# Kernel tuning notes

Measured on AMD Instinct MI355X. Metric: run time of the kernel, lower is better.

Reference implementation:

```python
import jax, jax.numpy as jnp
import numpy as np

EMBED = 768
HIDDEN = 768
HEADS = 12
HEAD_DIM = HIDDEN // HEADS
B, S = 4, 2048


def setup_inputs() -> dict:
    key = jax.random.key(0)
    ks = jax.random.split(key, 12)
    sd = 1.0 / np.sqrt(EMBED)
    return {
        "vector1": jax.random.normal(ks[0], (B, S, EMBED), jnp.float32),
        "vector2": jax.random.normal(ks[1], (B, S, EMBED), jnp.float32),
        "Wq": jax.random.normal(ks[2], (HIDDEN, EMBED), jnp.float32) * sd,
        "bq": jnp.zeros((HIDDEN,), jnp.float32),
        "Wk": jax.random.normal(ks[3], (HIDDEN, EMBED), jnp.float32) * sd,
        "bk": jnp.zeros((HIDDEN,), jnp.float32),
        "Wv": jax.random.normal(ks[4], (HIDDEN, EMBED), jnp.float32) * sd,
        "bv": jnp.zeros((HIDDEN,), jnp.float32),
        "Wo": jax.random.normal(ks[5], (EMBED, HIDDEN), jnp.float32) * sd,
        "bo": jnp.zeros((EMBED,), jnp.float32),
        "alpha": jnp.float32(0.5),
        "beta": jnp.float32(0.5),
    }


def reference(vector1, vector2, Wq, bq, Wk, bk, Wv, bv, Wo, bo, alpha, beta):
    b, s, _ = vector1.shape
    # Linear projections (torch Linear: x @ W.T + b)
    Q = (vector1 @ Wq.T + bq).reshape(b, s, HEADS, HEAD_DIM)  # [B,S,H,D]
    K = (vector2 @ Wk.T + bk).reshape(b, s, HEADS, HEAD_DIM)
    V = (vector2 @ Wv.T + bv).reshape(b, s, HEADS, HEAD_DIM)
    # NOTE: module scales by sqrt(hidden_dim), NOT sqrt(head_dim)
    scale = jnp.float32(np.sqrt(HIDDEN))
    scores = jnp.einsum("bqhd,bkhd->bhqk", Q / scale, K)  # [B,H,S,S]
    # max-subtract + softmax == numerically stable softmax
    attn = jax.nn.softmax(scores, axis=-1)
    out = jnp.einsum("bhqk,bkhd->bqhd", attn, V).reshape(b, s, HIDDEN)
    adjusted = vector1 @ Wo.T + bo
    return alpha * out + beta * adjusted
```

## Files before the change

### kernel.cpp

```cpp
#include <hip/hip_runtime.h>
#include <hip/hip_bf16.h>

#define LOG2E 1.4426950408889634f

typedef __attribute__((ext_vector_type(4)))  float f32x4;
typedef __attribute__((ext_vector_type(16))) float f32x16;
typedef __attribute__((ext_vector_type(8)))  short s16x8;
typedef __attribute__((ext_vector_type(8)))  unsigned short u16x8_t;
typedef __attribute__((ext_vector_type(4)))  int i32x4;

static __device__ __forceinline__ unsigned short f2b(float f) {
    __hip_bfloat16 h = __float2bfloat16(f);
    return __builtin_bit_cast(unsigned short, h);
}

static __device__ __forceinline__ void gload_lds16(const unsigned short* g, unsigned short* l) {
    __builtin_amdgcn_global_load_lds(
        (const __attribute__((address_space(1))) void*)g,
        (__attribute__((address_space(3))) void*)l, 16, 0, 0);
}

__global__ void cvt_f32_to_bf16(const float* __restrict__ src,
                                unsigned short* __restrict__ dst, int n4) {
    int i = blockIdx.x * blockDim.x + threadIdx.x;
    int stride = gridDim.x * blockDim.x;
    for (; i < n4; i += stride) {
        f32x4 v = reinterpret_cast<const f32x4*>(src)[i];
        ushort4 o;
        o.x = f2b(v.x); o.y = f2b(v.y); o.z = f2b(v.z); o.w = f2b(v.w);
        reinterpret_cast<ushort4*>(dst)[i] = o;
    }
}

__global__ void cvt_weights(const float* __restrict__ wq, const float* __restrict__ wk,
                            const float* __restrict__ wv, const float* __restrict__ wo,
                            unsigned short* __restrict__ dst, int quarter4) {
    int i = blockIdx.x * blockDim.x + threadIdx.x;
    int seg = i / quarter4;
    int j = i - seg * quarter4;
    const float* src = (seg == 0) ? wq : (seg == 1) ? wk : (seg == 2) ? wv : wo;
    f32x4 v = reinterpret_cast<const f32x4*>(src)[j];
    ushort4 o;
    o.x = f2b(v.x); o.y = f2b(v.y); o.z = f2b(v.z); o.w = f2b(v.w);
    reinterpret_cast<ushort4*>(dst)[i] = o;
}

__global__ __launch_bounds__(256) void gemm_qkvo(
    const unsigned short* __restrict__ A1,
    const unsigned short* __restrict__ A2,
    const unsigned short* __restrict__ Wcat,
    const float* __restrict__ bq, const float* __restrict__ bk,
    const float* __restrict__ bv, const float* __restrict__ bo,
    unsigned short* __restrict__ Qb,
    unsigned short* __restrict__ Kb,
    unsigned short* __restrict__ Vtb,
    float* __restrict__ adj,
    float qscale)
{
    __shared__ unsigned short As[128 * 64];
    __shared__ unsigned short Bs[128 * 64];

    const int n0g = blockIdx.x * 128;
    const int seg = blockIdx.x / 6;
    const int n0 = n0g - seg * 768;
    const int m0 = blockIdx.y * 128;
    const unsigned short* A = (seg == 1 || seg == 2) ? A2 : A1;
    const float* bias = (seg == 0) ? bq : (seg == 1) ? bk : (seg == 2) ? bv : bo;

    const int tid = threadIdx.x;
    const int w = tid >> 6, lane = tid & 63;
    const int lg = lane >> 4, lr = lane & 15;
    const int wm = w >> 1, wn = w & 1;
    const int srow = tid >> 3;
    const int scol = (tid & 7) * 8;

    const unsigned short* Ag = A    + (size_t)(m0  + srow) * 768 + scol;
    const unsigned short* Bg = Wcat + (size_t)(n0g + srow) * 768 + scol;
    unsigned short* Al = &As[tid * 8];
    unsigned short* Bl = &Bs[tid * 8];

    f32x4 acc[4][4];
#pragma unroll
    for (int i = 0; i < 4; i++)
#pragma unroll
        for (int j = 0; j < 4; j++) acc[i][j] = f32x4{0.f, 0.f, 0.f, 0.f};

    for (int k0 = 0; k0 < 768; k0 += 64) {
#pragma unroll
        for (int c = 0; c < 4; c++) {
            gload_lds16(Ag + c * 32 * 768 + k0, Al + c * 2048);
            gload_lds16(Bg + c * 32 * 768 + k0, Bl + c * 2048);
        }
        __syncthreads();
#pragma unroll
        for (int kk = 0; kk < 2; ++kk) {
            s16x8 af[4], bf[4];
#pragma unroll
            for (int mi = 0; mi < 4; mi++)
                af[mi] = *reinterpret_cast<const s16x8*>(&As[(wm * 64 + mi * 16 + lr) * 64 + kk * 32 + lg * 8]);
#pragma unroll
            for (int ni = 0; ni < 4; ni++)
                bf[ni] = *reinterpret_cast<const s16x8*>(&Bs[(wn * 64 + ni * 16 + lr) * 64 + kk * 32 + lg * 8]);
#pragma unroll
            for (int mi = 0; mi < 4; mi++)
#pragma unroll
                for (int ni = 0; ni < 4; ni++)
                    acc[mi][ni] = __builtin_amdgcn_mfma_f32_16x16x32_bf16(af[mi], bf[ni], acc[mi][ni], 0, 0, 0);
        }
        __syncthreads();
    }

#pragma unroll
    for (int ni = 0; ni < 4; ni++) {
        int n = n0 + wn * 64 + ni * 16 + lr;
        float bn = bias[n];
#pragma unroll
        for (int mi = 0; mi < 4; mi++) {
#pragma unroll
            for (int i = 0; i < 4; i++) {
                int m = m0 + wm * 64 + mi * 16 + 4 * lg + i;
                float v = acc[mi][ni][i] + bn;
                if (seg == 0) {
                    Qb[(size_t)m * 768 + n] = f2b(v * qscale);
                } else if (seg == 1) {
                    Kb[(size_t)m * 768 + n] = f2b(v);
                } else if (seg == 2) {
                    int bb = m >> 11, ss = m & 2047;
                    Vtb[((size_t)(bb * 768 + n) << 11) + ss] = f2b(v);
                } else {
                    adj[(size_t)m * 768 + n] = v;
                }
            }
        }
    }
}

__global__ __launch_bounds__(256) void attn_fused(
    const unsigned short* __restrict__ Qb,
    const unsigned short* __restrict__ Kb,
    const unsigned short* __restrict__ Vt,
    const float* __restrict__ adj,
    const float* __restrict__ alpha_p,
    const float* __restrict__ beta_p,
    float* __restrict__ out)
{
    __shared__ unsigned short Ksm[128][72];
    __shared__ unsigned short Vsm[64][136];

    const int bh = blockIdx.x;
    const int b = bh / 12, h = bh - 12 * (bh / 12);
    const int tid = threadIdx.x, w = tid >> 6, lane = tid & 63;
    const int ql = lane & 31, hi = lane >> 5;
    const int q0 = blockIdx.y * 128 + w * 32;

    const size_t qbase = ((size_t)(b * 2048 + q0 + ql)) * 768 + h * 64;
    s16x8 qreg[4];
#pragma unroll
    for (int ds = 0; ds < 4; ds++)
        qreg[ds] = *reinterpret_cast<const s16x8*>(Qb + qbase + ds * 16 + hi * 8);

    f32x16 acc[2];
#pragma unroll
    for (int dd = 0; dd < 2; dd++)
#pragma unroll
        for (int r = 0; r < 16; r++) acc[dd][r] = 0.f;
    float l = 0.f;

    const size_t kbase = (size_t)b * 2048 * 768 + (size_t)h * 64;
    const size_t vbase = (size_t)(b * 768 + h * 64) * 2048;

    const int krow = tid >> 3, kc8 = (tid & 7) * 8;
    const int vrow = tid >> 4, vc8 = (tid & 15) * 8;

    u16x8_t kst[4], vst[4];
    auto load_tile = [&](int t0) {
#pragma unroll
        for (int i = 0; i < 4; i++)
            kst[i] = *reinterpret_cast<const u16x8_t*>(Kb + kbase + (size_t)(t0 + i * 32 + krow) * 768 + kc8);
#pragma unroll
        for (int i = 0; i < 4; i++)
            vst[i] = *reinterpret_cast<const u16x8_t*>(Vt + vbase + (size_t)(i * 16 + vrow) * 2048 + t0 + vc8);
    };
    load_tile(0);

#pragma unroll 1
    for (int t0 = 0; t0 < 2048; t0 += 128) {
        __syncthreads();
#pragma unroll
        for (int i = 0; i < 4; i++)
            *reinterpret_cast<u16x8_t*>(&Ksm[i * 32 + krow][kc8]) = kst[i];
#pragma unroll
        for (int i = 0; i < 4; i++)
            *reinterpret_cast<u16x8_t*>(&Vsm[i * 16 + vrow][vc8]) = vst[i];
        __syncthreads();
        if (t0 + 128 < 2048) load_tile(t0 + 128);

#pragma unroll
        for (int kb2 = 0; kb2 < 4; kb2++) {
            f32x16 sc;
#pragma unroll
            for (int r = 0; r < 16; r++) sc[r] = 0.f;
#pragma unroll
            for (int ds = 0; ds < 4; ds++) {
                s16x8 ka = *reinterpret_cast<const s16x8*>(&Ksm[kb2 * 32 + ql][ds * 16 + hi * 8]);
                sc = __builtin_amdgcn_mfma_f32_32x32x16_bf16(ka, qreg[ds], sc, 0, 0, 0);
            }

            float p[16];
#pragma unroll
            for (int r = 0; r < 16; r++) p[r] = __builtin_exp2f(sc[r] * LOG2E);
            {
                float s0 = p[0] + p[1],  s1 = p[2] + p[3],  s2 = p[4] + p[5],  s3 = p[6] + p[7];
                float s4 = p[8] + p[9],  s5 = p[10] + p[11], s6 = p[12] + p[13], s7 = p[14] + p[15];
                float t0a = s0 + s1, t1a = s2 + s3, t2a = s4 + s5, t3a = s6 + s7;
                l += (t0a + t1a) + (t2a + t3a);
            }

            s16x8 pf[2];
            {
                unsigned int a0, b0, a1, b1, a2, b2, a3, b3;
                asm("v_cvt_pk_bf16_f32 %0, %1, %2" : "=v"(a0) : "v"(p[0]),  "v"(p[1]));
                asm("v_cvt_pk_bf16_f32 %0, %1, %2" : "=v"(b0) : "v"(p[4]),  "v"(p[5]));
                asm("v_cvt_pk_bf16_f32 %0, %1, %2" : "=v"(a1) : "v"(p[2]),  "v"(p[3]));
                asm("v_cvt_pk_bf16_f32 %0, %1, %2" : "=v"(b1) : "v"(p[6]),  "v"(p[7]));
                asm("v_cvt_pk_bf16_f32 %0, %1, %2" : "=v"(a2) : "v"(p[8]),  "v"(p[9]));
                asm("v_cvt_pk_bf16_f32 %0, %1, %2" : "=v"(b2) : "v"(p[12]), "v"(p[13]));
                asm("v_cvt_pk_bf16_f32 %0, %1, %2" : "=v"(a3) : "v"(p[10]), "v"(p[11]));
                asm("v_cvt_pk_bf16_f32 %0, %1, %2" : "=v"(b3) : "v"(p[14]), "v"(p[15]));
                asm volatile("v_permlane32_swap_b32 %0, %1" : "+v"(a0), "+v"(b0));
                asm volatile("v_permlane32_swap_b32 %0, %1" : "+v"(a1), "+v"(b1));
                asm volatile("v_permlane32_swap_b32 %0, %1" : "+v"(a2), "+v"(b2));
                asm volatile("v_permlane32_swap_b32 %0, %1" : "+v"(a3), "+v"(b3));
                i32x4 w0; w0[0] = (int)a0; w0[1] = (int)a1; w0[2] = (int)b0; w0[3] = (int)b1;
                i32x4 w1; w1[0] = (int)a2; w1[1] = (int)a3; w1[2] = (int)b2; w1[3] = (int)b3;
                pf[0] = __builtin_bit_cast(s16x8, w0);
                pf[1] = __builtin_bit_cast(s16x8, w1);
            }

#pragma unroll
            for (int ks = 0; ks < 2; ks++) {
#pragma unroll
                for (int dd = 0; dd < 2; dd++) {
                    s16x8 va = *reinterpret_cast<const s16x8*>(&Vsm[dd * 32 + ql][kb2 * 32 + ks * 16 + hi * 8]);
                    acc[dd] = __builtin_amdgcn_mfma_f32_32x32x16_bf16(va, pf[ks], acc[dd], 0, 0, 0);
                }
            }
        }
    }

    l += __shfl_xor(l, 32, 64);

    const float alpha = *alpha_p, beta = *beta_p;
    const float s = alpha / l;
#pragma unroll
    for (int dd = 0; dd < 2; dd++) {
#pragma unroll
        for (int rg = 0; rg < 4; rg++) {
            int d0 = dd * 32 + rg * 8 + hi * 4;
            size_t idx = qbase + d0;
            f32x4 av = *reinterpret_cast<const f32x4*>(adj + idx);
            f32x4 o;
#pragma unroll
            for (int i = 0; i < 4; i++)
                o[i] = acc[dd][rg * 4 + i] * s + beta * av[i];
            *reinterpret_cast<f32x4*>(out + idx) = o;
        }
    }
}

extern "C" void kernel_launch(void* const* d_in, const int* in_sizes, int n_in,
                              void* d_out, int out_size, void* d_ws, size_t ws_size,
                              hipStream_t stream) {
    const float* v1 = (const float*)d_in[0];
    const float* v2 = (const float*)d_in[1];
    const float* Wq = (const float*)d_in[2];
    const float* bq = (const float*)d_in[3];
    const float* Wk = (const float*)d_in[4];
    const float* bk = (const float*)d_in[5];
    const float* Wv = (const float*)d_in[6];
    const float* bv = (const float*)d_in[7];
    const float* Wo = (const float*)d_in[8];
    const float* bo = (const float*)d_in[9];
    const float* alpha = (const float*)d_in[10];
    const float* beta = (const float*)d_in[11];
    float* out = (float*)d_out;

    const size_t ACT = (size_t)8192 * 768;
    const size_t WSZ = (size_t)768 * 768;
    char* ws = (char*)d_ws;
    size_t off = 0;
    auto alloc = [&](size_t bytes) {
        char* p = ws + off;
        off += (bytes + 255) & ~(size_t)255;
        return p;
    };
    unsigned short* v1b  = (unsigned short*)alloc(ACT * 2);
    unsigned short* v2b  = (unsigned short*)alloc(ACT * 2);
    unsigned short* wcat = (unsigned short*)alloc(4 * WSZ * 2);
    unsigned short* Qb   = (unsigned short*)alloc(ACT * 2);
    unsigned short* Kb   = (unsigned short*)alloc(ACT * 2);
    unsigned short* Vtb  = (unsigned short*)alloc(ACT * 2);
    float* adj = (float*)alloc(ACT * 4);

    cvt_f32_to_bf16<<<dim3(1024), dim3(256), 0, stream>>>(v1, v1b, (int)(ACT / 4));
    cvt_f32_to_bf16<<<dim3(1024), dim3(256), 0, stream>>>(v2, v2b, (int)(ACT / 4));
    cvt_weights<<<dim3((int)(4 * WSZ / 4 / 256)), dim3(256), 0, stream>>>(
        Wq, Wk, Wv, Wo, wcat, (int)(WSZ / 4));

    const float qscale = 0.03608439182435161f;
    gemm_qkvo<<<dim3(24, 64), dim3(256), 0, stream>>>(
        v1b, v2b, wcat, bq, bk, bv, bo, Qb, Kb, Vtb, adj, qscale);

    attn_fused<<<dim3(48, 16), dim3(256), 0, stream>>>(Qb, Kb, Vtb, adj, alpha, beta, out);
}
```

Measured before the change: 304.4 us.

## Double-buffer K/V tiles in attention, fold log2e into Q scale, raise occupancy

The attention kernel now uses two 64-key LDS buffers for K and V instead of one 128-key tile. The next tile is written into the spare buffer while the current one is consumed, which leaves one barrier per iteration instead of two. The log2(e) factor is folded into the Q projection scale so the per-score multiply before exp2 goes away. The change also adds launch_bounds minimum blocks of 3 and s_setprio around the MFMA groups to raise occupancy and favour matrix issue, at the cost of more loop iterations and possible register pressure.

```diff
diff --git a/kernel.cpp b/kernel.cpp
--- a/kernel.cpp
+++ b/kernel.cpp
@@ -135,7 +135,7 @@
     }
 }
 
-__global__ __launch_bounds__(256) void attn_fused(
+__global__ __launch_bounds__(256, 3) void attn_fused(
     const unsigned short* __restrict__ Qb,
     const unsigned short* __restrict__ Kb,
     const unsigned short* __restrict__ Vt,
@@ -144,8 +144,8 @@
     const float* __restrict__ beta_p,
     float* __restrict__ out)
 {
-    __shared__ unsigned short Ksm[128][72];
-    __shared__ unsigned short Vsm[64][136];
+    __shared__ unsigned short Ksm[2][64][72];
+    __shared__ unsigned short Vsm[2][64][72];
 
     const int bh = blockIdx.x;
     const int b = bh / 12, h = bh - 12 * (bh / 12);
@@ -159,56 +159,65 @@
     for (int ds = 0; ds < 4; ds++)
         qreg[ds] = *reinterpret_cast<const s16x8*>(Qb + qbase + ds * 16 + hi * 8);
 
+    f32x16 z16;
+#pragma unroll
+    for (int r = 0; r < 16; r++) z16[r] = 0.f;
     f32x16 acc[2];
 #pragma unroll
-    for (int dd = 0; dd < 2; dd++)
-#pragma unroll
-        for (int r = 0; r < 16; r++) acc[dd][r] = 0.f;
+    for (int dd = 0; dd < 2; dd++) acc[dd] = z16;
     float l = 0.f;
 
     const size_t kbase = (size_t)b * 2048 * 768 + (size_t)h * 64;
     const size_t vbase = (size_t)(b * 768 + h * 64) * 2048;
 
     const int krow = tid >> 3, kc8 = (tid & 7) * 8;
-    const int vrow = tid >> 4, vc8 = (tid & 15) * 8;
-
-    u16x8_t kst[4], vst[4];
+    const int vrow = tid >> 3, vc8 = (tid & 7) * 8;
+
+    u16x8_t kst[2], vst[2];
     auto load_tile = [&](int t0) {
 #pragma unroll
-        for (int i = 0; i < 4; i++)
+        for (int i = 0; i < 2; i++)
             kst[i] = *reinterpret_cast<const u16x8_t*>(Kb + kbase + (size_t)(t0 + i * 32 + krow) * 768 + kc8);
 #pragma unroll
-        for (int i = 0; i < 4; i++)
-            vst[i] = *reinterpret_cast<const u16x8_t*>(Vt + vbase + (size_t)(i * 16 + vrow) * 2048 + t0 + vc8);
+        for (int i = 0; i < 2; i++)
+            vst[i] = *reinterpret_cast<const u16x8_t*>(Vt + vbase + (size_t)(i * 32 + vrow) * 2048 + t0 + vc8);
     };
+    auto write_tile = [&](int buf) {
+#pragma unroll
+        for (int i = 0; i < 2; i++)
+            *reinterpret_cast<u16x8_t*>(&Ksm[buf][i * 32 + krow][kc8]) = kst[i];
+#pragma unroll
+        for (int i = 0; i < 2; i++)
+            *reinterpret_cast<u16x8_t*>(&Vsm[buf][i * 32 + vrow][vc8]) = vst[i];
+    };
+
     load_tile(0);
+    write_tile(0);
+    load_tile(64);
+    __syncthreads();
 
 #pragma unroll 1
-    for (int t0 = 0; t0 < 2048; t0 += 128) {
-        __syncthreads();
-#pragma unroll
-        for (int i = 0; i < 4; i++)
-            *reinterpret_cast<u16x8_t*>(&Ksm[i * 32 + krow][kc8]) = kst[i];
-#pragma unroll
-        for (int i = 0; i < 4; i++)
-            *reinterpret_cast<u16x8_t*>(&Vsm[i * 16 + vrow][vc8]) = vst[i];
-        __syncthreads();
-        if (t0 + 128 < 2048) load_tile(t0 + 128);
-
-#pragma unroll
-        for (int kb2 = 0; kb2 < 4; kb2++) {
-            f32x16 sc;
-#pragma unroll
-            for (int r = 0; r < 16; r++) sc[r] = 0.f;
-#pragma unroll
-            for (int ds = 0; ds < 4; ds++) {
-                s16x8 ka = *reinterpret_cast<const s16x8*>(&Ksm[kb2 * 32 + ql][ds * 16 + hi * 8]);
-                sc = __builtin_amdgcn_mfma_f32_32x32x16_bf16(ka, qreg[ds], sc, 0, 0, 0);
-            }
+    for (int t = 0; t < 32; t++) {
+        const int cur = t & 1;
+        if (t + 1 < 32) write_tile(cur ^ 1);
+        if (t + 2 < 32) load_tile((t + 2) * 64);
+
+#pragma unroll
+        for (int kb2 = 0; kb2 < 2; kb2++) {
+            s16x8 ka0 = *reinterpret_cast<const s16x8*>(&Ksm[cur][kb2 * 32 + ql][0 * 16 + hi * 8]);
+            s16x8 ka1 = *reinterpret_cast<const s16x8*>(&Ksm[cur][kb2 * 32 + ql][1 * 16 + hi * 8]);
+            s16x8 ka2 = *reinterpret_cast<const s16x8*>(&Ksm[cur][kb2 * 32 + ql][2 * 16 + hi * 8]);
+            s16x8 ka3 = *reinterpret_cast<const s16x8*>(&Ksm[cur][kb2 * 32 + ql][3 * 16 + hi * 8]);
+            __builtin_amdgcn_s_setprio(1);
+            f32x16 sc = __builtin_amdgcn_mfma_f32_32x32x16_bf16(ka0, qreg[0], z16, 0, 0, 0);
+            sc = __builtin_amdgcn_mfma_f32_32x32x16_bf16(ka1, qreg[1], sc, 0, 0, 0);
+            sc = __builtin_amdgcn_mfma_f32_32x32x16_bf16(ka2, qreg[2], sc, 0, 0, 0);
+            sc = __builtin_amdgcn_mfma_f32_32x32x16_bf16(ka3, qreg[3], sc, 0, 0, 0);
+            __builtin_amdgcn_s_setprio(0);
 
             float p[16];
 #pragma unroll
-            for (int r = 0; r < 16; r++) p[r] = __builtin_exp2f(sc[r] * LOG2E);
+            for (int r = 0; r < 16; r++) p[r] = __builtin_exp2f(sc[r]);
             {
                 float s0 = p[0] + p[1],  s1 = p[2] + p[3],  s2 = p[4] + p[5],  s3 = p[6] + p[7];
                 float s4 = p[8] + p[9],  s5 = p[10] + p[11], s6 = p[12] + p[13], s7 = p[14] + p[15];
@@ -237,15 +246,18 @@
                 pf[1] = __builtin_bit_cast(s16x8, w1);
             }
 
-#pragma unroll
-            for (int ks = 0; ks < 2; ks++) {
-#pragma unroll
-                for (int dd = 0; dd < 2; dd++) {
-                    s16x8 va = *reinterpret_cast<const s16x8*>(&Vsm[dd * 32 + ql][kb2 * 32 + ks * 16 + hi * 8]);
-                    acc[dd] = __builtin_amdgcn_mfma_f32_32x32x16_bf16(va, pf[ks], acc[dd], 0, 0, 0);
-                }
-            }
-        }
+            s16x8 va00 = *reinterpret_cast<const s16x8*>(&Vsm[cur][0 * 32 + ql][kb2 * 32 + 0 * 16 + hi * 8]);
+            s16x8 va01 = *reinterpret_cast<const s16x8*>(&Vsm[cur][1 * 32 + ql][kb2 * 32 + 0 * 16 + hi * 8]);
+            s16x8 va10 = *reinterpret_cast<const s16x8*>(&Vsm[cur][0 * 32 + ql][kb2 * 32 + 1 * 16 + hi * 8]);
+            s16x8 va11 = *reinterpret_cast<const s16x8*>(&Vsm[cur][1 * 32 + ql][kb2 * 32 + 1 * 16 + hi * 8]);
+            __builtin_amdgcn_s_setprio(1);
+            acc[0] = __builtin_amdgcn_mfma_f32_32x32x16_bf16(va00, pf[0], acc[0], 0, 0, 0);
+            acc[1] = __builtin_amdgcn_mfma_f32_32x32x16_bf16(va01, pf[0], acc[1], 0, 0, 0);
+            acc[0] = __builtin_amdgcn_mfma_f32_32x32x16_bf16(va10, pf[1], acc[0], 0, 0, 0);
+            acc[1] = __builtin_amdgcn_mfma_f32_32x32x16_bf16(va11, pf[1], acc[1], 0, 0, 0);
+            __builtin_amdgcn_s_setprio(0);
+        }
+        __syncthreads();
     }
 
     l += __shfl_xor(l, 32, 64);
@@ -307,7 +319,7 @@
     cvt_weights<<<dim3((int)(4 * WSZ / 4 / 256)), dim3(256), 0, stream>>>(
         Wq, Wk, Wv, Wo, wcat, (int)(WSZ / 4));
 
-    const float qscale = 0.03608439182435161f;
+    const float qscale = 0.03608439182435161f * 1.4426950408889634f;
     gemm_qkvo<<<dim3(24, 64), dim3(256), 0, stream>>>(
         v1b, v2b, wcat, bq, bk, bv, bo, Qb, Kb, Vtb, adj, qscale);
 
```

New measurement: 289.6 us. 4.9% less time.
